# Optimization experiments

Measured on AMD Instinct MI355X. Metric: run time of the kernel, lower is better.

The kernel has to match this reference:

```python
import jax, jax.numpy as jnp
import numpy as np

B, T, C, H = 4, 2048, 1024, 16
HS = C // H  # head size = 64


def setup_inputs() -> dict:
    key = jax.random.key(0)
    ks = jax.random.split(key, 9)
    s = 1.0 / np.sqrt(C)
    return {
        "x": jax.random.normal(ks[0], (B, T, C), dtype=jnp.float32),
        "Wq": jax.random.uniform(ks[1], (C, C), jnp.float32, -s, s),
        "bq": jax.random.uniform(ks[2], (C,), jnp.float32, -s, s),
        "Wk": jax.random.uniform(ks[3], (C, C), jnp.float32, -s, s),
        "bk": jax.random.uniform(ks[4], (C,), jnp.float32, -s, s),
        "Wv": jax.random.uniform(ks[5], (C, C), jnp.float32, -s, s),
        "bv": jax.random.uniform(ks[6], (C,), jnp.float32, -s, s),
        "Wp": jax.random.uniform(ks[7], (C, C), jnp.float32, -s, s),
        "bp": jax.random.uniform(ks[8], (C,), jnp.float32, -s, s),
    }


def reference(x, Wq, bq, Wk, bk, Wv, bv, Wp, bp):
    Bx, Tx, Cx = x.shape
    # QKV projections -> [B, H, T, HS]
    def heads(w, b):
        return (x @ w.T + b).reshape(Bx, Tx, H, HS).transpose(0, 2, 1, 3)
    q = heads(Wq, bq)
    k = heads(Wk, bk)
    v = heads(Wv, bv)
    scale = 1.0 / np.sqrt(HS).astype(np.float32)
    att = jnp.einsum("bhqd,bhkd->bhqk", q, k) * scale  # [B,H,T,T]
    causal = jnp.tril(jnp.ones((Tx, Tx), dtype=bool))
    att = jnp.where(causal[None, None], att, -jnp.inf)
    att = jax.nn.softmax(att, axis=-1)
    y = jnp.einsum("bhqk,bhkd->bhqd", att, v)  # [B,H,T,HS]
    y = y.transpose(0, 2, 1, 3).reshape(Bx, Tx, Cx)
    return y @ Wp.T + bp
```

## Files before the change

kernel.cpp:

```cpp
#include <hip/hip_runtime.h>
#include <hip/hip_bf16.h>

typedef __hip_bfloat16 bf16;
typedef __attribute__((ext_vector_type(8))) short bf16x8;
typedef __attribute__((ext_vector_type(4))) float f32x4;

#define B_  4
#define T_  2048
#define C_  1024
#define H_  16
#define HS_ 64
#define M_  (B_ * T_)

__device__ __forceinline__ short f2bf(float x) {
    bf16 h = __float2bfloat16(x);
    return *reinterpret_cast<short*>(&h);
}
__device__ __forceinline__ unsigned pk2(float lo, float hi) {
    return ((unsigned)(unsigned short)f2bf(hi) << 16) | (unsigned short)f2bf(lo);
}

__device__ __forceinline__ unsigned pk2a(float lo, float hi) {
    unsigned r;
    asm("v_cvt_pk_bf16_f32 %0, %1, %2" : "=v"(r) : "v"(lo), "v"(hi));
    return r;
}

__device__ __forceinline__ float fast_exp2(float x) {
#if __has_builtin(__builtin_amdgcn_exp2f)
    return __builtin_amdgcn_exp2f(x);
#else
    return exp2f(x);
#endif
}

__device__ __forceinline__ void async16(void* lds, const void* g) {
    __builtin_amdgcn_global_load_lds(
        (const __attribute__((address_space(1))) unsigned int*)g,
        (__attribute__((address_space(3))) unsigned int*)lds, 16, 0, 0);
}

#define CV_S0 1048576u
#define CV_S1 (CV_S0 + 393216u)
#define CV_S2 (CV_S1 + 131072u)
#define CV_S3 (CV_S2 + 384u)

__global__ __launch_bounds__(256) void convert_kernel(
    const float* __restrict__ x,
    const float* __restrict__ Wq, const float* __restrict__ Wk,
    const float* __restrict__ Wv, const float* __restrict__ Wp,
    const float* __restrict__ bq, const float* __restrict__ bk,
    const float* __restrict__ bv,
    bf16* __restrict__ xb, bf16* __restrict__ wqkv, bf16* __restrict__ wpb,
    float* __restrict__ bqkv)
{
    const unsigned idx = blockIdx.x * 256u + threadIdx.x;
    if (idx >= CV_S3) return;

    const float* src;
    bf16* dst;
    size_t soff, doff;
    if (idx < CV_S0) {
        soff = (size_t)idx * 8; doff = soff; src = x; dst = xb;
    } else if (idx < CV_S1) {
        const size_t e0 = (size_t)(idx - CV_S0) * 8;
        const int row = (int)(e0 >> 10);
        const int col = (int)(e0 & 1023);
        src = (row < 1024) ? Wq : (row < 2048) ? Wk : Wv;
        soff = ((size_t)(row & 1023) << 10) + col;
        doff = e0; dst = wqkv;
    } else if (idx < CV_S2) {
        soff = (size_t)(idx - CV_S1) * 8; doff = soff; src = Wp; dst = wpb;
    } else {
        const int e0 = (int)(idx - CV_S2) * 8;
        #pragma unroll
        for (int e = 0; e < 8; e++) {
            const int n = e0 + e;
            bqkv[n] = (n < 1024) ? bq[n] : (n < 2048) ? bk[n - 1024] : bv[n - 2048];
        }
        return;
    }

    const float4 a = *(const float4*)(src + soff);
    const float4 b = *(const float4*)(src + soff + 4);
    uint4 o;
    o.x = pk2(a.x, a.y);
    o.y = pk2(a.z, a.w);
    o.z = pk2(b.x, b.y);
    o.w = pk2(b.z, b.w);
    *(uint4*)(dst + doff) = o;
}

template <int QKV>
__global__ __launch_bounds__(256) void gemm_mfma(const bf16* __restrict__ A,
                                                 const bf16* __restrict__ W,
                                                 const float* __restrict__ bias,
                                                 bf16* __restrict__ qo,
                                                 bf16* __restrict__ ko,
                                                 bf16* __restrict__ vo,
                                                 float* __restrict__ out)
{
    __shared__ __align__(16) short As[128 * 64];
    __shared__ __align__(16) short Bs[128 * 64];

    const int tid  = threadIdx.x;
    const int lane = tid & 63;
    const int w    = tid >> 6;
    const int l15  = lane & 15;
    const int quad = lane >> 4;
    const int xs = (blockIdx.x & 7) * ((int)gridDim.x >> 3) + (blockIdx.x >> 3);
    const int m0 = xs * 128;
    const int n0 = blockIdx.y * 128;
    const int wm = (w & 1) * 64;
    const int wn = (w >> 1) * 64;

    f32x4 acc[4][4];
    #pragma unroll
    for (int i = 0; i < 4; i++)
        #pragma unroll
        for (int j = 0; j < 4; j++)
            acc[i][j] = (f32x4){0.f, 0.f, 0.f, 0.f};

    const int srow   = lane >> 3;
    const int schunk = (lane & 7) ^ srow;

    for (int k0 = 0; k0 < C_; k0 += 64) {
        #pragma unroll
        for (int i = 0; i < 4; i++) {
            const int r0 = w * 32 + i * 8;
            async16(&As[r0 * 64],
                    A + (size_t)(m0 + r0 + srow) * C_ + k0 + schunk * 8);
            async16(&Bs[r0 * 64],
                    W + (size_t)(n0 + r0 + srow) * C_ + k0 + schunk * 8);
        }
        __syncthreads();

        #pragma unroll
        for (int kc = 0; kc < 2; kc++) {
            const int swz = ((kc * 4 + quad) ^ (l15 & 7)) * 8;
            bf16x8 af[4], bfr[4];
            #pragma unroll
            for (int mi = 0; mi < 4; mi++)
                af[mi] = *(const bf16x8*)&As[(wm + mi * 16 + l15) * 64 + swz];
            #pragma unroll
            for (int ni = 0; ni < 4; ni++)
                bfr[ni] = *(const bf16x8*)&Bs[(wn + ni * 16 + l15) * 64 + swz];
            #pragma unroll
            for (int mi = 0; mi < 4; mi++)
                #pragma unroll
                for (int ni = 0; ni < 4; ni++)
                    acc[mi][ni] = __builtin_amdgcn_mfma_f32_16x16x32_bf16(
                        af[mi], bfr[ni], acc[mi][ni], 0, 0, 0);
        }
        __syncthreads();
    }

    #pragma unroll
    for (int mi = 0; mi < 4; mi++) {
        #pragma unroll
        for (int r = 0; r < 4; r++) {
            const int m  = m0 + wm + mi * 16 + quad * 4 + r;
            const int bb = m >> 11;
            const int tt = m & (T_ - 1);
            #pragma unroll
            for (int ni = 0; ni < 4; ni++) {
                const int n = n0 + wn + ni * 16 + l15;
                const float val = acc[mi][ni][r] + bias[n];
                if (QKV) {
                    const int sel = n >> 10;
                    const int nn  = n & 1023;
                    const int hh  = nn >> 6;
                    const int dd  = nn & 63;
                    bf16* dst = (sel == 0) ? qo : (sel == 1) ? ko : vo;
                    dst[(((size_t)(bb * H_ + hh) * T_ + tt) << 6) + dd] =
                        __float2bfloat16(val);
                } else {
                    out[((size_t)m << 10) + n] = val;
                }
            }
        }
    }
}

__global__ __launch_bounds__(256) void transpose_v(const bf16* __restrict__ V,
                                                   bf16* __restrict__ Vt)
{
    __shared__ __align__(16) short tile[64 * 72];

    const int t0 = blockIdx.x * 64;
    const int h = blockIdx.y, b = blockIdx.z;
    const size_t base = ((size_t)(b * H_ + h) * T_) << 6;

    const int tr = threadIdx.x & 63;
    const int dc = (threadIdx.x >> 6) * 16;
    const bf16x8 a = *(const bf16x8*)(V + base + (size_t)(t0 + tr) * 64 + dc);
    const bf16x8 c = *(const bf16x8*)(V + base + (size_t)(t0 + tr) * 64 + dc + 8);
    #pragma unroll
    for (int e = 0; e < 8; e++) {
        tile[(dc + e) * 72 + tr]     = a[e];
        tile[(dc + 8 + e) * 72 + tr] = c[e];
    }
    __syncthreads();

    const int d  = threadIdx.x >> 2;
    const int tc = (threadIdx.x & 3) * 16;
    const bf16x8 o0 = *(const bf16x8*)&tile[d * 72 + tc];
    const bf16x8 o1 = *(const bf16x8*)&tile[d * 72 + tc + 8];
    *(bf16x8*)(Vt + base + (size_t)d * T_ + t0 + tc)     = o0;
    *(bf16x8*)(Vt + base + (size_t)d * T_ + t0 + tc + 8) = o1;
}

#define LOG2E_X_SCALE 0.18033688011112042f
#define LOG2E_X_BIAS  -34.62468098133513f

__global__ __launch_bounds__(256) void attn_bal(const bf16* __restrict__ Q,
                                                const bf16* __restrict__ K,
                                                const bf16* __restrict__ Vt,
                                                bf16* __restrict__ Y)
{
    __shared__ __align__(16) short Pl[4][64 * 72];
    __shared__ __align__(16) short Ks[2][64 * 64];
    __shared__ __align__(16) short Vs[2][64 * 64];

    const int tid  = threadIdx.x;
    const int lane = tid & 63;
    const int w    = tid >> 6;
    const int l15  = lane & 15;
    const int quad = lane >> 4;

    const unsigned bid  = blockIdx.x;
    const unsigned orig = ((bid & 7u) << 6) | (bid >> 3);
    const int bx = orig & 7;
    const int h  = (orig >> 3) & 15;
    const int b  = (int)(orig >> 7);
    const size_t base = ((size_t)(b * H_ + h) * T_) << 6;

    const int g  = bx * 4 + w;
    const int qf = g * 32;
    const int qm = T_ - 32 - qf;
    const int r0[4] = {qf, qf + 16, qm, qm + 16};
    const int ntf = ((qf + 31) >> 6) + 1;
    const int ntm = ((qm + 31) >> 6) + 1;
    const int ntmax = ((2047 - 128 * bx) >> 6) + 1;

    bf16x8 qfr[4][2];
    #pragma unroll
    for (int qn = 0; qn < 4; qn++)
        #pragma unroll
        for (int ch = 0; ch < 2; ch++)
            qfr[qn][ch] = *(const bf16x8*)(Q + base +
                (size_t)(r0[qn] + l15) * 64 + ch * 32 + quad * 8);

    f32x4 acc[4][4];
    #pragma unroll
    for (int dt = 0; dt < 4; dt++)
        #pragma unroll
        for (int qn = 0; qn < 4; qn++)
            acc[dt][qn] = (f32x4){0.f, 0.f, 0.f, 0.f};
    float lsum[4] = {0.f, 0.f, 0.f, 0.f};

    short* myP = &Pl[w][0];

    const int srow   = lane >> 3;
    const int schunk = (lane & 7) ^ srow;
    const int myrow  = l15 & 7;

    #pragma unroll
    for (int i = 0; i < 2; i++) {
        const int r0s = w * 16 + i * 8;
        async16(&Ks[0][r0s * 64],
                K + base + (size_t)(r0s + srow) * 64 + schunk * 8);
        async16(&Vs[0][r0s * 64],
                Vt + base + (size_t)(r0s + srow) * T_ + schunk * 8);
    }
    __syncthreads();

    int cur = 0;
    for (int t = 0; t < ntmax; t++) {
        const int j0 = t << 6;

        if (t + 1 < ntmax) {
            const int j0n = j0 + 64;
            #pragma unroll
            for (int i = 0; i < 2; i++) {
                const int r0s = w * 16 + i * 8;
                async16(&Ks[cur ^ 1][r0s * 64],
                        K + base + (size_t)(j0n + r0s + srow) * 64 + schunk * 8);
                async16(&Vs[cur ^ 1][r0s * 64],
                        Vt + base + (size_t)(r0s + srow) * T_ + j0n + schunk * 8);
            }
        }

        if (t < ntm) {
            const bool fact = (t < ntf);

            #pragma unroll
            for (int kt = 0; kt < 4; kt++) {
                const int krow = (kt * 16 + l15) * 64;
                const bf16x8 kf0 = *(const bf16x8*)&Ks[cur][krow + ((quad ^ myrow) * 8)];
                const bf16x8 kf1 = *(const bf16x8*)&Ks[cur][krow + (((4 + quad) ^ myrow) * 8)];
                #pragma unroll
                for (int qn = 0; qn < 4; qn++) {
                    if (qn < 2 && !fact) continue;
                    f32x4 s = (f32x4){0.f, 0.f, 0.f, 0.f};
                    s = __builtin_amdgcn_mfma_f32_16x16x32_bf16(kf0, qfr[qn][0], s, 0, 0, 0);
                    s = __builtin_amdgcn_mfma_f32_16x16x32_bf16(kf1, qfr[qn][1], s, 0, 0, 0);
                    const int r0q = r0[qn];
                    const bool msk = (j0 + 63 > r0q);
                    float p[4];
                    #pragma unroll
                    for (int r = 0; r < 4; r++) {
                        float e = fast_exp2(fmaf(s[r], LOG2E_X_SCALE, LOG2E_X_BIAS));
                        if (msk) {
                            const int key = j0 + kt * 16 + quad * 4 + r;
                            e = (key <= r0q + l15) ? e : 0.f;
                        }
                        p[r] = e;
                        lsum[qn] += e;
                    }
                    uint2 pkd;
                    pkd.x = pk2a(p[0], p[1]);
                    pkd.y = pk2a(p[2], p[3]);
                    *(uint2*)&myP[(qn * 16 + l15) * 72 + kt * 16 + quad * 4] = pkd;
                }
            }

            #pragma unroll
            for (int ch = 0; ch < 2; ch++) {
                bf16x8 pf[4];
                #pragma unroll
                for (int qn = 0; qn < 4; qn++)
                    if (qn >= 2 || fact)
                        pf[qn] = *(const bf16x8*)&myP[(qn * 16 + l15) * 72 + ch * 32 + quad * 8];
                #pragma unroll
                for (int dt = 0; dt < 4; dt++) {
                    const bf16x8 vf = *(const bf16x8*)
                        &Vs[cur][(dt * 16 + l15) * 64 + (((ch * 4 + quad) ^ myrow) * 8)];
                    #pragma unroll
                    for (int qn = 0; qn < 4; qn++)
                        if (qn >= 2 || fact)
                            acc[dt][qn] = __builtin_amdgcn_mfma_f32_16x16x32_bf16(
                                vf, pf[qn], acc[dt][qn], 0, 0, 0);
                }
            }
        }

        __syncthreads();
        cur ^= 1;
    }

    #pragma unroll
    for (int qn = 0; qn < 4; qn++) {
        lsum[qn] += __shfl_xor(lsum[qn], 16, 64);
        lsum[qn] += __shfl_xor(lsum[qn], 32, 64);
    }

    #pragma unroll
    for (int qn = 0; qn < 4; qn++) {
        const float inv = 1.f / lsum[qn];
        const int tt = r0[qn] + l15;
        bf16* yrow = Y + (((size_t)(b * T_ + tt)) << 10) + (h << 6);
        #pragma unroll
        for (int dt = 0; dt < 4; dt++) {
            uint2 o;
            o.x = pk2a(acc[dt][qn][0] * inv, acc[dt][qn][1] * inv);
            o.y = pk2a(acc[dt][qn][2] * inv, acc[dt][qn][3] * inv);
            *(uint2*)(yrow + dt * 16 + quad * 4) = o;
        }
    }
}

__global__ void zero_out_kernel(float* out, size_t n) {
    const size_t i = (size_t)blockIdx.x * 256 + threadIdx.x;
    if (i < n) out[i] = 0.f;
}

extern "C" void kernel_launch(void* const* d_in, const int* in_sizes, int n_in,
                              void* d_out, int out_size, void* d_ws, size_t ws_size,
                              hipStream_t stream)
{
    const float* x  = (const float*)d_in[0];
    const float* Wq = (const float*)d_in[1];
    const float* bq = (const float*)d_in[2];
    const float* Wk = (const float*)d_in[3];
    const float* bk = (const float*)d_in[4];
    const float* Wv = (const float*)d_in[5];
    const float* bv = (const float*)d_in[6];
    const float* Wp = (const float*)d_in[7];
    const float* bp = (const float*)d_in[8];

    const size_t nElem = (size_t)M_ * C_;

    size_t off = 0;
    auto alloc = [&](size_t bytes) {
        void* p = (char*)d_ws + off;
        off += (bytes + 255) & ~(size_t)255;
        return p;
    };
    bf16*  xb   = (bf16*)alloc(nElem * 2);
    bf16*  q    = (bf16*)alloc(nElem * 2);
    bf16*  k    = (bf16*)alloc(nElem * 2);
    bf16*  v    = (bf16*)alloc(nElem * 2);
    bf16*  wqkv = (bf16*)alloc((size_t)3 * C_ * C_ * 2);
    bf16*  wpb  = (bf16*)alloc((size_t)C_ * C_ * 2);
    float* bqkv = (float*)alloc(3 * C_ * 4);

    if (off > ws_size) {
        const size_t n = (size_t)out_size;
        zero_out_kernel<<<(int)((n + 255) / 256), 256, 0, stream>>>((float*)d_out, n);
        return;
    }

    convert_kernel<<<(CV_S3 + 255) / 256, 256, 0, stream>>>(
        x, Wq, Wk, Wv, Wp, bq, bk, bv, xb, wqkv, wpb, bqkv);

    gemm_mfma<1><<<dim3(M_ / 128, 3 * C_ / 128), 256, 0, stream>>>(
        xb, wqkv, bqkv, q, k, v, nullptr);

    bf16* vt = xb;
    transpose_v<<<dim3(T_ / 64, H_, B_), 256, 0, stream>>>(v, vt);

    bf16* y = v;
    attn_bal<<<dim3(512), 256, 0, stream>>>(q, k, vt, y);

    gemm_mfma<0><<<dim3(M_ / 128, C_ / 128), 256, 0, stream>>>(
        y, wpb, bp, nullptr, nullptr, nullptr, (float*)d_out);
}
```

Baseline: 276.4 us.

## Fuse V transpose into QKV GEMM epilogue via shared-memory staging

The QKV GEMM's V-column tiles now stage their biased bf16 results in shared memory, transposed, and write V directly in [B,H,HS,T] layout. This removes the separate transpose_v kernel launch and its extra global read and write of V. In exchange, the V-tile blocks take an extra LDS round trip and two barriers per head half. Y now reuses the xb buffer.

```diff
diff --git a/kernel.cpp b/kernel.cpp
--- a/kernel.cpp
+++ b/kernel.cpp
@@ -100,8 +100,9 @@
                                                  bf16* __restrict__ vo,
                                                  float* __restrict__ out)
 {
-    __shared__ __align__(16) short As[128 * 64];
-    __shared__ __align__(16) short Bs[128 * 64];
+    __shared__ __align__(16) short smem[2 * 128 * 64];
+    short* As = smem;
+    short* Bs = smem + 128 * 64;
 
     const int tid  = threadIdx.x;
     const int lane = tid & 63;
@@ -155,6 +156,46 @@
         __syncthreads();
     }
 
+    const int selB = n0 >> 10;
+
+    if (QKV && selB == 2) {
+        short* epi = smem;
+        const int myhalf = (wn != 0);
+        const int bb  = m0 >> 11;
+        const int tt0 = m0 & (T_ - 1);
+        #pragma unroll
+        for (int h0 = 0; h0 < 2; h0++) {
+            if (myhalf == h0) {
+                #pragma unroll
+                for (int ni = 0; ni < 4; ni++) {
+                    const int nl = ni * 16 + l15;
+                    const float bv_ = bias[n0 + wn + nl];
+                    #pragma unroll
+                    for (int mi = 0; mi < 4; mi++) {
+                        const int mlb = wm + mi * 16 + quad * 4;
+                        *(unsigned*)&epi[nl * 136 + mlb] =
+                            pk2a(acc[mi][ni][0] + bv_, acc[mi][ni][1] + bv_);
+                        *(unsigned*)&epi[nl * 136 + mlb + 2] =
+                            pk2a(acc[mi][ni][2] + bv_, acc[mi][ni][3] + bv_);
+                    }
+                }
+            }
+            __syncthreads();
+            const int rr = tid >> 2;
+            const int q4 = tid & 3;
+            const int hh = ((n0 & 1023) >> 6) + h0;
+            bf16* dst = vo + ((size_t)((bb * H_ + hh) * 64 + rr) << 11)
+                           + tt0 + q4 * 32;
+            #pragma unroll
+            for (int c = 0; c < 4; c++) {
+                const bf16x8 vv = *(const bf16x8*)&epi[rr * 136 + q4 * 32 + c * 8];
+                *(bf16x8*)(dst + c * 8) = vv;
+            }
+            __syncthreads();
+        }
+        return;
+    }
+
     #pragma unroll
     for (int mi = 0; mi < 4; mi++) {
         #pragma unroll
@@ -167,11 +208,10 @@
                 const int n = n0 + wn + ni * 16 + l15;
                 const float val = acc[mi][ni][r] + bias[n];
                 if (QKV) {
-                    const int sel = n >> 10;
                     const int nn  = n & 1023;
                     const int hh  = nn >> 6;
                     const int dd  = nn & 63;
-                    bf16* dst = (sel == 0) ? qo : (sel == 1) ? ko : vo;
+                    bf16* dst = (selB == 0) ? qo : ko;
                     dst[(((size_t)(bb * H_ + hh) * T_ + tt) << 6) + dd] =
                         __float2bfloat16(val);
                 } else {
@@ -180,34 +220,6 @@
             }
         }
     }
-}
-
-__global__ __launch_bounds__(256) void transpose_v(const bf16* __restrict__ V,
-                                                   bf16* __restrict__ Vt)
-{
-    __shared__ __align__(16) short tile[64 * 72];
-
-    const int t0 = blockIdx.x * 64;
-    const int h = blockIdx.y, b = blockIdx.z;
-    const size_t base = ((size_t)(b * H_ + h) * T_) << 6;
-
-    const int tr = threadIdx.x & 63;
-    const int dc = (threadIdx.x >> 6) * 16;
-    const bf16x8 a = *(const bf16x8*)(V + base + (size_t)(t0 + tr) * 64 + dc);
-    const bf16x8 c = *(const bf16x8*)(V + base + (size_t)(t0 + tr) * 64 + dc + 8);
-    #pragma unroll
-    for (int e = 0; e < 8; e++) {
-        tile[(dc + e) * 72 + tr]     = a[e];
-        tile[(dc + 8 + e) * 72 + tr] = c[e];
-    }
-    __syncthreads();
-
-    const int d  = threadIdx.x >> 2;
-    const int tc = (threadIdx.x & 3) * 16;
-    const bf16x8 o0 = *(const bf16x8*)&tile[d * 72 + tc];
-    const bf16x8 o1 = *(const bf16x8*)&tile[d * 72 + tc + 8];
-    *(bf16x8*)(Vt + base + (size_t)d * T_ + t0 + tc)     = o0;
-    *(bf16x8*)(Vt + base + (size_t)d * T_ + t0 + tc + 8) = o1;
 }
 
 #define LOG2E_X_SCALE 0.18033688011112042f
@@ -400,7 +412,7 @@
     bf16*  xb   = (bf16*)alloc(nElem * 2);
     bf16*  q    = (bf16*)alloc(nElem * 2);
     bf16*  k    = (bf16*)alloc(nElem * 2);
-    bf16*  v    = (bf16*)alloc(nElem * 2);
+    bf16*  vtb  = (bf16*)alloc(nElem * 2);
     bf16*  wqkv = (bf16*)alloc((size_t)3 * C_ * C_ * 2);
     bf16*  wpb  = (bf16*)alloc((size_t)C_ * C_ * 2);
     float* bqkv = (float*)alloc(3 * C_ * 4);
@@ -415,13 +427,10 @@
         x, Wq, Wk, Wv, Wp, bq, bk, bv, xb, wqkv, wpb, bqkv);
 
     gemm_mfma<1><<<dim3(M_ / 128, 3 * C_ / 128), 256, 0, stream>>>(
-        xb, wqkv, bqkv, q, k, v, nullptr);
-
-    bf16* vt = xb;
-    transpose_v<<<dim3(T_ / 64, H_, B_), 256, 0, stream>>>(v, vt);
-
-    bf16* y = v;
-    attn_bal<<<dim3(512), 256, 0, stream>>>(q, k, vt, y);
+        xb, wqkv, bqkv, q, k, vtb, nullptr);
+
+    bf16* y = xb;
+    attn_bal<<<dim3(512), 256, 0, stream>>>(q, k, vtb, y);
 
     gemm_mfma<0><<<dim3(M_ / 128, C_ / 128), 256, 0, stream>>>(
         y, wpb, bp, nullptr, nullptr, nullptr, (float*)d_out);
```

New measurement: 268.0 us. -3.0%, faster.
